# Kernel tuning notes

Hardware: AMD Instinct MI355X
Metric: run time of the kernel (lower is better)

Reference implementation:

```python
import math
import jax, jax.numpy as jnp
import numpy as np

D = 768      # hidden_size
H = 16       # num_attention_heads (hardcoded in module)
DH = D // H  # value dim per head
SEQ = 512    # fpos/tpos are taken modulo 512
EPS = 1e-5   # torch LayerNorm default
SCALE = math.sqrt(D / H)  # attention_head_size = dim_key_query_all / num_heads


def _collab_attn(h, fpos, tpos, Wq, Wk, Wcb, Wv, bv, mix, Wd, bd, lng, lnb):
    """CollaborativeAttention.forward on one segment. h: [SEQ, D]."""
    fpos = fpos % SEQ
    tpos = tpos % SEQ
    fs = h[fpos]                                   # [F, D] gathered 'from' nodes
    ts = h[tpos]                                   # [T, D] gathered 'to' nodes
    q = fs @ Wq.T                                  # [F, D] (no bias)
    k = ts @ Wk.T                                  # [T, D] (no bias)
    mq = q[None, :, :] * mix[:, None, :]           # [H, F, D] per-head mixing
    scores = jnp.einsum('hfd,td->hft', mq, k)      # [H, F, T] full-D contraction
    cb = (ts @ Wcb.T).T                            # [H, T] content bias
    scores = (scores + cb[:, None, :]) / SCALE
    probs = jax.nn.softmax(scores, axis=-1)        # dropout = identity at eval
    v = (ts @ Wv.T + bv).reshape(-1, H, DH).transpose(1, 0, 2)  # [H, T, DH]
    ctx = jnp.einsum('hft,htd->hfd', probs, v)     # [H, F, DH]
    ctx = ctx.transpose(1, 0, 2).reshape(-1, D) @ Wd.T + bd      # [F, D]
    x = fs + ctx                                   # residual on gathered nodes
    mu = x.mean(-1, keepdims=True)
    var = ((x - mu) ** 2).mean(-1, keepdims=True)
    return lng * (x - mu) / jnp.sqrt(var + EPS) + lnb


def _encoder(hidden_states, fpos, tpos, qtoc, ctoq):
    outs = []
    for b in range(3):  # fixed small segment count, matches original unrolling
        o1 = _collab_attn(hidden_states[b], fpos[b], tpos[b], *qtoc).mean(0)
        o2 = _collab_attn(hidden_states[b], tpos[b], fpos[b], *ctoq).mean(0)
        outs.append(jnp.concatenate([o1, o2]))
    return jnp.stack(outs)  # [3, 2*D]


def setup_inputs() -> dict:
    key = jax.random.key(0)
    ks = jax.random.split(key, 32)
    inp = {
        'hidden_states': jax.random.normal(ks[0], (3, SEQ, D), jnp.float32),
        'fpos': jax.random.randint(ks[1], (3, 2048), 0, SEQ, jnp.int32),
        'tpos': jax.random.randint(ks[2], (3, 2048), 0, SEQ, jnp.int32),
    }
    i = 3
    for p in ('qtoc', 'ctoq'):
        for n, shape, std in (('Wq', (D, D), 0.02), ('Wk', (D, D), 0.02),
                              ('Wcb', (H, D), 0.02), ('Wv', (D, D), 0.02),
                              ('Wd', (D, D), 0.02), ('mix', (H, D), 0.2)):
            inp[p + '_' + n] = std * jax.random.normal(ks[i], shape, jnp.float32)
            i += 1
        inp[p + '_bv'] = jnp.zeros((D,), jnp.float32)
        inp[p + '_bd'] = jnp.zeros((D,), jnp.float32)
        inp[p + '_lng'] = jnp.ones((D,), jnp.float32)
        inp[p + '_lnb'] = jnp.zeros((D,), jnp.float32)
    return inp


def reference(hidden_states, fpos, tpos,
              qtoc_Wq, qtoc_Wk, qtoc_Wcb, qtoc_Wv, qtoc_Wd, qtoc_mix,
              qtoc_bv, qtoc_bd, qtoc_lng, qtoc_lnb,
              ctoq_Wq, ctoq_Wk, ctoq_Wcb, ctoq_Wv, ctoq_Wd, ctoq_mix,
              ctoq_bv, ctoq_bd, ctoq_lng, ctoq_lnb):
    qtoc = (qtoc_Wq, qtoc_Wk, qtoc_Wcb, qtoc_Wv, qtoc_bv, qtoc_mix,
            qtoc_Wd, qtoc_bd, qtoc_lng, qtoc_lnb)
    ctoq = (ctoq_Wq, ctoq_Wk, ctoq_Wcb, ctoq_Wv, ctoq_bv, ctoq_mix,
            ctoq_Wd, ctoq_bd, ctoq_lng, ctoq_lnb)
    return _encoder(hidden_states, fpos, tpos, qtoc, ctoq)
```

## Files before the change

kernel.cpp:

```cpp
#include <hip/hip_runtime.h>
#include <math.h>

#define DD 768
#define HH 16
#define DHH 48
#define NPOS 512
#define NIDX 2048
#define INV_SCALE 0.14433756729740643f
#define LN_EPS 1e-5f

typedef __bf16 bf16_t;
typedef __bf16 bf16x8 __attribute__((ext_vector_type(8)));
typedef float f32x4 __attribute__((ext_vector_type(4)));

__device__ __forceinline__ void g2lds16(const void* g, void* l) {
  __builtin_amdgcn_global_load_lds((const __attribute__((address_space(1))) void*)g,
                                   (__attribute__((address_space(3))) void*)l, 16, 0, 0);
}

struct CvtDesc { const float* src; bf16_t* dst; int n8; };
struct CvtBatch { CvtDesc d[9]; };

__global__ __launch_bounds__(256) void prep(const int* __restrict__ fpos,
                                            const int* __restrict__ tpos,
                                            int* __restrict__ CNT, CvtBatch cvb,
                                            const float* __restrict__ hs,
                                            const float* __restrict__ Wcb0,
                                            const float* __restrict__ Wcb1,
                                            float* __restrict__ cbG) {
  const int bid = blockIdx.x;
  const int tid = threadIdx.x;
  __shared__ int shist[NPOS];
  if (bid < 6) {
    const int b = bid >> 1, which = bid & 1;
    const int* src = (which ? tpos : fpos) + b * NIDX;
    for (int i = tid; i < NPOS; i += 256) shist[i] = 0;
    __syncthreads();
    for (int i = tid; i < NIDX; i += 256) atomicAdd(&shist[src[i] & (NPOS - 1)], 1);
    __syncthreads();
    for (int i = tid; i < NPOS; i += 256) CNT[bid * NPOS + i] = shist[i];
  } else if (bid < 582) {
    const CvtDesc de = cvb.d[(bid - 6) >> 6];
    for (int i = ((bid - 6) & 63) * 256 + tid; i < de.n8; i += 64 * 256) {
      const f32x4 a = *(const f32x4*)(de.src + (size_t)i * 8);
      const f32x4 b = *(const f32x4*)(de.src + (size_t)i * 8 + 4);
      bf16_t t[8];
#pragma unroll
      for (int e = 0; e < 4; ++e) { t[e] = (bf16_t)a[e]; t[4 + e] = (bf16_t)b[e]; }
      *(bf16x8*)(de.dst + (size_t)i * 8) = *(bf16x8*)t;
    }
  } else {
    const int g = bid - 582;
    const int pd = g >> 5, t0 = (g & 31) * 16;
    const int b = pd >> 1;
    const float* W = (pd & 1) ? Wcb1 : Wcb0;
    const int tl = tid >> 4, hh = tid & 15;
    const float* hrow = hs + ((size_t)b * NPOS + t0 + tl) * DD;
    const float* wrow = W + hh * DD;
    float s = 0.f;
    for (int k = 0; k < DD; k += 4) {
      const f32x4 a = *(const f32x4*)(hrow + k);
      const f32x4 bq = *(const f32x4*)(wrow + k);
      s += a[0] * bq[0] + a[1] * bq[1] + a[2] * bq[2] + a[3] * bq[3];
    }
    cbG[((size_t)pd * NPOS + t0 + tl) * HH + hh] = s;
  }
}

struct MDesc { const bf16_t* A; const bf16_t* B; const float* bias; void* C; int out_bf16; };
struct MBatch { MDesc d[18]; };

__global__ __launch_bounds__(256, 2) void mfma_gemm(MBatch batch) {
  const MDesc de = batch.d[blockIdx.y];
  const int mt = blockIdx.x & 3, nt = blockIdx.x >> 2;
  const int m0 = mt * 128, n0 = nt * 128;

  __shared__ bf16_t At[4096];
  __shared__ bf16_t Bt[4096];

  const int tid = threadIdx.x;
  const int w = tid >> 6, lane = tid & 63;
  const int wm = w >> 1, wn = w & 1;
  const int lm = lane & 15, lq = lane >> 4;

  f32x4 acc[4][4] = {};

  for (int k0 = 0; k0 < 768; k0 += 32) {
    __syncthreads();
    {
      const int lqq = lane & 3, lr = lane >> 2;
#pragma unroll
      for (int i = 0; i < 2; ++i) {
        const int issue = w + i * 4;
        const int row = issue * 16 + lr;
        g2lds16(de.A + (size_t)(m0 + row) * 768 + k0 + lqq * 8, At + issue * 512);
        g2lds16(de.B + (size_t)(n0 + row) * 768 + k0 + lqq * 8, Bt + issue * 512);
      }
    }
    __syncthreads();
    bf16x8 af[4], bfr[4];
#pragma unroll
    for (int f = 0; f < 4; ++f) {
      af[f] = *(const bf16x8*)(At + (wm * 64 + f * 16 + lm) * 32 + lq * 8);
      bfr[f] = *(const bf16x8*)(Bt + (wn * 64 + f * 16 + lm) * 32 + lq * 8);
    }
#pragma unroll
    for (int i = 0; i < 4; ++i)
#pragma unroll
      for (int j = 0; j < 4; ++j)
        acc[i][j] = __builtin_amdgcn_mfma_f32_16x16x32_bf16(af[i], bfr[j], acc[i][j], 0, 0, 0);
  }

#pragma unroll
  for (int i = 0; i < 4; ++i) {
    const int rbase = m0 + wm * 64 + i * 16 + lq * 4;
#pragma unroll
    for (int j = 0; j < 4; ++j) {
      const int c = n0 + wn * 64 + j * 16 + lm;
      const float bv = de.bias ? de.bias[c] : 0.f;
#pragma unroll
      for (int r = 0; r < 4; ++r) {
        const float v = acc[i][j][r] + bv;
        if (de.out_bf16) ((bf16_t*)de.C)[(size_t)(rbase + r) * 768 + c] = (bf16_t)v;
        else             ((float*)de.C)[(size_t)(rbase + r) * 768 + c] = v;
      }
    }
  }
}

__global__ __launch_bounds__(256) void vtrans(const bf16_t* __restrict__ V,
                                              bf16_t* __restrict__ Vt) {
  const int g = blockIdx.x;
  const int tt = g & 15;
  const int rem = g >> 4;
  const int dt = rem % 24, pd = rem / 24;
  const int t0 = tt * 32, d0 = dt * 32;
  __shared__ bf16_t tile[32][34];
  const int c = threadIdx.x & 31, r0 = threadIdx.x >> 5;
#pragma unroll
  for (int i = 0; i < 4; ++i) {
    const int r = r0 + i * 8;
    tile[c][r] = V[((size_t)pd * NPOS + t0 + r) * DD + d0 + c];
  }
  __syncthreads();
#pragma unroll
  for (int i = 0; i < 4; ++i) {
    const int r = r0 + i * 8;
    Vt[((size_t)pd * DD + d0 + r) * NPOS + t0 + c] = tile[r][c];
  }
}

__global__ __launch_bounds__(256, 3) void attn_mfma(
    const bf16_t* __restrict__ Qg, const bf16_t* __restrict__ Kg,
    const bf16_t* __restrict__ Vt, const float* __restrict__ cbG,
    const int* __restrict__ CNT, const float* __restrict__ mix0,
    const float* __restrict__ mix1, bf16_t* __restrict__ CTX) {
  const int bid = blockIdx.x;
  const int ft = bid & 7, h = (bid >> 3) & 15, pd = bid >> 7;
  const int dir = pd & 1;
  const int f0 = ft * 64;

  __shared__ bf16_t At[64 * 32];
  __shared__ bf16_t Bt[128 * 32];
  __shared__ bf16_t P[64 * 136];
  __shared__ bf16_t Vs[64 * 136];
  __shared__ float mixs[768];
  __shared__ float cbw[512];
  __shared__ float rowl[64];

  const int tid = threadIdx.x;
  const int w = tid >> 6, lane = tid & 63;
  const bf16_t* Qp = Qg + (size_t)pd * NPOS * DD;
  const bf16_t* Kp = Kg + (size_t)pd * NPOS * DD;
  const bf16_t* Vp = Vt + (size_t)pd * DD * NPOS + (size_t)h * DHH * NPOS;
  const float* mix = (dir ? mix1 : mix0) + h * DD;
  const int* cnt = CNT + ((pd & ~1) + (1 - dir)) * NPOS;

  for (int i = tid; i < 768; i += 256) mixs[i] = mix[i];
  for (int i = tid; i < 512; i += 256)
    cbw[i] = cbG[((size_t)pd * NPOS + i) * HH + h] * INV_SCALE + __logf((float)cnt[i]);
  for (int i = tid; i < 16 * 136; i += 256) {
    const int r = i / 136, c = i % 136;
    Vs[(48 + r) * 136 + c] = (bf16_t)((r == 0 && c < 128) ? 1.f : 0.f);
  }
  __syncthreads();

  const int wm = w >> 1, wn = w & 1;
  const int lm = lane & 15, lq = lane >> 4;
  const int sr = lane >> 2, sq = lane & 3;

  f32x4 pv[4] = {};

  for (int jt = 0; jt < 4; ++jt) {
    const int j0 = jt * 128;
    f32x4 sa[2][4] = {};

    for (int k0 = 0; k0 < DD; k0 += 32) {
      __syncthreads();
#pragma unroll
      for (int c = 0; c < 3; ++c) {
        const int issue = w + c * 4;
        if (issue < 4)
          g2lds16(Qp + (size_t)(f0 + issue * 16 + sr) * DD + k0 + sq * 8, At + issue * 512);
        else {
          const int e = issue - 4;
          g2lds16(Kp + (size_t)(j0 + e * 16 + sr) * DD + k0 + sq * 8, Bt + e * 512);
        }
      }
      __syncthreads();
      const f32x4 mxa = *(const f32x4*)&mixs[k0 + lq * 8];
      const f32x4 mxb = *(const f32x4*)&mixs[k0 + lq * 8 + 4];
      bf16x8 af[2], bfr[4];
#pragma unroll
      for (int i = 0; i < 2; ++i) {
        const bf16x8 q = *(const bf16x8*)(At + (wm * 32 + i * 16 + lm) * 32 + lq * 8);
        bf16_t t[8];
#pragma unroll
        for (int e = 0; e < 4; ++e) {
          t[e]     = (bf16_t)((float)q[e] * mxa[e]);
          t[4 + e] = (bf16_t)((float)q[4 + e] * mxb[e]);
        }
        af[i] = *(bf16x8*)t;
      }
#pragma unroll
      for (int j = 0; j < 4; ++j)
        bfr[j] = *(const bf16x8*)(Bt + (wn * 64 + j * 16 + lm) * 32 + lq * 8);
#pragma unroll
      for (int i = 0; i < 2; ++i)
#pragma unroll
        for (int j = 0; j < 4; ++j)
          sa[i][j] = __builtin_amdgcn_mfma_f32_16x16x32_bf16(af[i], bfr[j], sa[i][j], 0, 0, 0);
    }
    __syncthreads();

#pragma unroll
    for (int j = 0; j < 4; ++j) {
      const int col = wn * 64 + j * 16 + lm;
      const float cb = cbw[j0 + col];
#pragma unroll
      for (int i = 0; i < 2; ++i) {
        const int rbase = wm * 32 + i * 16 + lq * 4;
#pragma unroll
        for (int r = 0; r < 4; ++r)
          P[(rbase + r) * 136 + col] = (bf16_t)__expf(sa[i][j][r] * INV_SCALE + cb);
      }
    }
    for (int i = tid; i < 48 * 16; i += 256) {
      const int r = i >> 4, cc = i & 15;
      *(bf16x8*)(Vs + r * 136 + cc * 8) = *(const bf16x8*)(Vp + (size_t)r * NPOS + j0 + cc * 8);
    }
    __syncthreads();

#pragma unroll
    for (int kk = 0; kk < 4; ++kk) {
      const bf16x8 pa = *(const bf16x8*)(P + (w * 16 + lm) * 136 + kk * 32 + lq * 8);
#pragma unroll
      for (int j = 0; j < 4; ++j) {
        const bf16x8 pb = *(const bf16x8*)(Vs + (j * 16 + lm) * 136 + kk * 32 + lq * 8);
        pv[j] = __builtin_amdgcn_mfma_f32_16x16x32_bf16(pa, pb, pv[j], 0, 0, 0);
      }
    }
  }

  if (lm == 0) {
#pragma unroll
    for (int r = 0; r < 4; ++r) rowl[w * 16 + lq * 4 + r] = pv[3][r];
  }
  __syncthreads();
#pragma unroll
  for (int j = 0; j < 3; ++j) {
#pragma unroll
    for (int r = 0; r < 4; ++r) {
      const int fr = w * 16 + lq * 4 + r;
      CTX[((size_t)pd * NPOS + f0 + fr) * DD + h * DHH + j * 16 + lm] =
          (bf16_t)(pv[j][r] / rowl[fr]);
    }
  }
}

__global__ __launch_bounds__(256) void ln_mean_kernel(
    const float* __restrict__ hs, const float* __restrict__ XB,
    const int* __restrict__ CNT,
    const float* __restrict__ lng0, const float* __restrict__ lnb0,
    const float* __restrict__ lng1, const float* __restrict__ lnb1,
    float* __restrict__ out) {
  const int blk = blockIdx.x;
  const int chunk = blk & 15;
  const int pd = blk >> 4;
  const int b = pd >> 1, dir = pd & 1;
  const float* lng = dir ? lng1 : lng0;
  const float* lnb = dir ? lnb1 : lnb0;
  const int* cnt = CNT + pd * NPOS;
  const float* hb = hs + (size_t)b * NPOS * DD;
  const float* xb = XB + (size_t)pd * NPOS * DD;

  __shared__ float wacc[4][DD];
  const int tid = threadIdx.x;
  const int wave = tid >> 6, lane = tid & 63;
  for (int d0 = tid; d0 < 4 * DD; d0 += 256) ((float*)wacc)[d0] = 0.f;
  __syncthreads();

  float lg[12], lb[12];
#pragma unroll
  for (int qd = 0; qd < 12; ++qd) {
    lg[qd] = lng[lane + qd * 64];
    lb[qd] = lnb[lane + qd * 64];
  }

  for (int rr = 0; rr < 8; ++rr) {
    const int p = chunk * 32 + wave * 8 + rr;
    float x[12];
    float s = 0.f, ss = 0.f;
#pragma unroll
    for (int qd = 0; qd < 12; ++qd) {
      const int d0 = lane + qd * 64;
      const float xv = hb[(size_t)p * DD + d0] + xb[(size_t)p * DD + d0];
      x[qd] = xv; s += xv; ss += xv * xv;
    }
#pragma unroll
    for (int o = 1; o < 64; o <<= 1) {
      s += __shfl_xor(s, o);
      ss += __shfl_xor(ss, o);
    }
    const float mu = s * (1.f / 768.f);
    const float var = ss * (1.f / 768.f) - mu * mu;
    const float rstd = rsqrtf(var + LN_EPS);
    const float wgt = (float)cnt[p];
    if (wgt != 0.f) {
#pragma unroll
      for (int qd = 0; qd < 12; ++qd) {
        const int d0 = lane + qd * 64;
        wacc[wave][d0] += wgt * (lg[qd] * (x[qd] - mu) * rstd + lb[qd]);
      }
    }
  }
  __syncthreads();
  for (int d0 = tid; d0 < DD; d0 += 256) {
    const float t = wacc[0][d0] + wacc[1][d0] + wacc[2][d0] + wacc[3][d0];
    atomicAdd(&out[b * 1536 + dir * 768 + d0], t * (1.f / 2048.f));
  }
}

extern "C" void kernel_launch(void* const* d_in, const int* in_sizes, int n_in,
                              void* d_out, int out_size, void* d_ws, size_t ws_size,
                              hipStream_t stream) {
  const float* hs  = (const float*)d_in[0];
  const int* fpos  = (const int*)d_in[1];
  const int* tpos  = (const int*)d_in[2];

  const float* Wq[2]; const float* Wk[2]; const float* Wcb[2]; const float* Wv[2];
  const float* Wd[2]; const float* mixp[2];
  const float* bv[2]; const float* bd[2]; const float* lng[2]; const float* lnb[2];
  for (int p = 0; p < 2; ++p) {
    const int base = 3 + p * 10;
    Wq[p]   = (const float*)d_in[base + 0];
    Wk[p]   = (const float*)d_in[base + 1];
    Wcb[p]  = (const float*)d_in[base + 2];
    Wv[p]   = (const float*)d_in[base + 3];
    Wd[p]   = (const float*)d_in[base + 4];
    mixp[p] = (const float*)d_in[base + 5];
    bv[p]   = (const float*)d_in[base + 6];
    bd[p]   = (const float*)d_in[base + 7];
    lng[p]  = (const float*)d_in[base + 8];
    lnb[p]  = (const float*)d_in[base + 9];
  }

  char* wsp = (char*)d_ws;
  size_t off = 0;
  auto alloc = [&](size_t bytes) { char* p = wsp + off; off = (off + bytes + 255) & ~(size_t)255; return p; };
  bf16_t* hsb  = (bf16_t*)alloc((size_t)3 * NPOS * DD * 2);
  bf16_t* Wb   = (bf16_t*)alloc((size_t)8 * DD * DD * 2);
  bf16_t* Qbf  = (bf16_t*)alloc((size_t)6 * NPOS * DD * 2);
  bf16_t* Kbf  = (bf16_t*)alloc((size_t)6 * NPOS * DD * 2);
  bf16_t* Vbf  = (bf16_t*)alloc((size_t)6 * NPOS * DD * 2);
  bf16_t* VtG  = (bf16_t*)alloc((size_t)6 * DD * NPOS * 2);
  bf16_t* CTXb = (bf16_t*)alloc((size_t)6 * NPOS * DD * 2);
  float*  XB   = (float*) alloc((size_t)6 * NPOS * DD * 4);
  float*  cbG  = (float*) alloc((size_t)6 * NPOS * HH * 4);
  int*    CNTb = (int*)   alloc((size_t)6 * NPOS * 4);

  hipMemsetAsync(d_out, 0, (size_t)out_size * sizeof(float), stream);

  CvtBatch cvb{};
  cvb.d[0] = CvtDesc{hs, hsb, 3 * NPOS * DD / 8};
  const float* wsrc[8] = {Wq[0], Wk[0], Wv[0], Wd[0], Wq[1], Wk[1], Wv[1], Wd[1]};
  for (int i = 0; i < 8; ++i)
    cvb.d[1 + i] = CvtDesc{wsrc[i], Wb + (size_t)i * DD * DD, DD * DD / 8};
  prep<<<774, 256, 0, stream>>>(fpos, tpos, CNTb, cvb, hs, Wcb[0], Wcb[1], cbG);

  MBatch gb{};
  int n = 0;
  for (int b = 0; b < 3; ++b)
    for (int p = 0; p < 2; ++p) {
      const int pd = b * 2 + p;
      const bf16_t* A = hsb + (size_t)b * NPOS * DD;
      const size_t o = (size_t)pd * NPOS * DD;
      gb.d[n++] = MDesc{A, Wb + (size_t)(p * 4 + 0) * DD * DD, nullptr, Qbf + o, 1};
      gb.d[n++] = MDesc{A, Wb + (size_t)(p * 4 + 1) * DD * DD, nullptr, Kbf + o, 1};
      gb.d[n++] = MDesc{A, Wb + (size_t)(p * 4 + 2) * DD * DD, bv[p],   Vbf + o, 1};
    }
  mfma_gemm<<<dim3(24, 18), 256, 0, stream>>>(gb);

  vtrans<<<2304, 256, 0, stream>>>(Vbf, VtG);

  attn_mfma<<<768, 256, 0, stream>>>(Qbf, Kbf, VtG, cbG, CNTb, mixp[0], mixp[1], CTXb);

  MBatch gd{};
  for (int b = 0; b < 3; ++b)
    for (int p = 0; p < 2; ++p) {
      const int pd = b * 2 + p;
      const size_t o = (size_t)pd * NPOS * DD;
      gd.d[pd] = MDesc{CTXb + o, Wb + (size_t)(p * 4 + 3) * DD * DD, bd[p], XB + o, 0};
    }
  mfma_gemm<<<dim3(24, 6), 256, 0, stream>>>(gd);

  ln_mean_kernel<<<96, 256, 0, stream>>>(hs, XB, CNTb, lng[0], lnb[0], lng[1], lnb[1],
                                         (float*)d_out);
}
```

Measured before the change: 286.1 us.

## Double-buffer GEMM and attention loads, fuse V transpose, shrink tiles and LDS

The GEMM tile shrinks to 64x128 and both GEMM and attention score loops now double-buffer their global-to-LDS loads, issuing the next k-slice before computing the current one. The V projection writes its output already transposed, which removes the separate vtrans kernel and the Vbf buffer. Attention LDS is packed into one union buffer, allowing 4 blocks per CU, and the softmax scale is folded into the mix vector. The aim is to hide load latency, raise occupancy and cut one launch plus a memory round-trip, at the cost of strided scattered stores for the transposed V output.

```diff
diff --git a/kernel.cpp b/kernel.cpp
--- a/kernel.cpp
+++ b/kernel.cpp
@@ -67,53 +67,62 @@
   }
 }
 
-struct MDesc { const bf16_t* A; const bf16_t* B; const float* bias; void* C; int out_bf16; };
+struct MDesc { const bf16_t* A; const bf16_t* B; const float* bias; void* C; int mode; };
 struct MBatch { MDesc d[18]; };
 
-__global__ __launch_bounds__(256, 2) void mfma_gemm(MBatch batch) {
+__global__ __launch_bounds__(256, 4) void gemm64(MBatch batch) {
   const MDesc de = batch.d[blockIdx.y];
-  const int mt = blockIdx.x & 3, nt = blockIdx.x >> 2;
-  const int m0 = mt * 128, n0 = nt * 128;
-
-  __shared__ bf16_t At[4096];
-  __shared__ bf16_t Bt[4096];
+  const int mt = blockIdx.x & 7, nt = blockIdx.x >> 3;
+  const int m0 = mt * 64, n0 = nt * 128;
+
+  __shared__ bf16_t SA[2][2048];
+  __shared__ bf16_t SB[2][4096];
 
   const int tid = threadIdx.x;
   const int w = tid >> 6, lane = tid & 63;
   const int wm = w >> 1, wn = w & 1;
   const int lm = lane & 15, lq = lane >> 4;
-
-  f32x4 acc[4][4] = {};
-
-  for (int k0 = 0; k0 < 768; k0 += 32) {
-    __syncthreads();
-    {
-      const int lqq = lane & 3, lr = lane >> 2;
-#pragma unroll
-      for (int i = 0; i < 2; ++i) {
-        const int issue = w + i * 4;
-        const int row = issue * 16 + lr;
-        g2lds16(de.A + (size_t)(m0 + row) * 768 + k0 + lqq * 8, At + issue * 512);
-        g2lds16(de.B + (size_t)(n0 + row) * 768 + k0 + lqq * 8, Bt + issue * 512);
-      }
-    }
-    __syncthreads();
-    bf16x8 af[4], bfr[4];
-#pragma unroll
-    for (int f = 0; f < 4; ++f) {
-      af[f] = *(const bf16x8*)(At + (wm * 64 + f * 16 + lm) * 32 + lq * 8);
-      bfr[f] = *(const bf16x8*)(Bt + (wn * 64 + f * 16 + lm) * 32 + lq * 8);
-    }
-#pragma unroll
-    for (int i = 0; i < 4; ++i)
+  const int sr = lane >> 2, sq = lane & 3;
+
+  f32x4 acc[2][4] = {};
+
+  auto stage = [&](int buf, int k0) {
+#pragma unroll
+    for (int c = 0; c < 3; ++c) {
+      const int issue = w + c * 4;
+      if (issue < 4)
+        g2lds16(de.A + (size_t)(m0 + issue * 16 + sr) * 768 + k0 + sq * 8,
+                SA[buf] + issue * 512);
+      else {
+        const int e = issue - 4;
+        g2lds16(de.B + (size_t)(n0 + e * 16 + sr) * 768 + k0 + sq * 8,
+                SB[buf] + e * 512);
+      }
+    }
+  };
+
+  stage(0, 0);
+  for (int k0i = 0; k0i < 24; ++k0i) {
+    const int cur = k0i & 1;
+    __syncthreads();
+    if (k0i + 1 < 24) stage(cur ^ 1, (k0i + 1) * 32);
+    bf16x8 af[2], bfr[4];
+#pragma unroll
+    for (int i = 0; i < 2; ++i)
+      af[i] = *(const bf16x8*)(SA[cur] + (wm * 32 + i * 16 + lm) * 32 + lq * 8);
+#pragma unroll
+    for (int j = 0; j < 4; ++j)
+      bfr[j] = *(const bf16x8*)(SB[cur] + (wn * 64 + j * 16 + lm) * 32 + lq * 8);
+#pragma unroll
+    for (int i = 0; i < 2; ++i)
 #pragma unroll
       for (int j = 0; j < 4; ++j)
         acc[i][j] = __builtin_amdgcn_mfma_f32_16x16x32_bf16(af[i], bfr[j], acc[i][j], 0, 0, 0);
   }
 
 #pragma unroll
-  for (int i = 0; i < 4; ++i) {
-    const int rbase = m0 + wm * 64 + i * 16 + lq * 4;
+  for (int i = 0; i < 2; ++i) {
+    const int rbase = m0 + wm * 32 + i * 16 + lq * 4;
 #pragma unroll
     for (int j = 0; j < 4; ++j) {
       const int c = n0 + wn * 64 + j * 16 + lm;
@@ -121,36 +130,15 @@
 #pragma unroll
       for (int r = 0; r < 4; ++r) {
         const float v = acc[i][j][r] + bv;
-        if (de.out_bf16) ((bf16_t*)de.C)[(size_t)(rbase + r) * 768 + c] = (bf16_t)v;
-        else             ((float*)de.C)[(size_t)(rbase + r) * 768 + c] = v;
-      }
-    }
-  }
-}
-
-__global__ __launch_bounds__(256) void vtrans(const bf16_t* __restrict__ V,
-                                              bf16_t* __restrict__ Vt) {
-  const int g = blockIdx.x;
-  const int tt = g & 15;
-  const int rem = g >> 4;
-  const int dt = rem % 24, pd = rem / 24;
-  const int t0 = tt * 32, d0 = dt * 32;
-  __shared__ bf16_t tile[32][34];
-  const int c = threadIdx.x & 31, r0 = threadIdx.x >> 5;
-#pragma unroll
-  for (int i = 0; i < 4; ++i) {
-    const int r = r0 + i * 8;
-    tile[c][r] = V[((size_t)pd * NPOS + t0 + r) * DD + d0 + c];
-  }
-  __syncthreads();
-#pragma unroll
-  for (int i = 0; i < 4; ++i) {
-    const int r = r0 + i * 8;
-    Vt[((size_t)pd * DD + d0 + r) * NPOS + t0 + c] = tile[r][c];
-  }
-}
-
-__global__ __launch_bounds__(256, 3) void attn_mfma(
+        if (de.mode == 0)      ((float*)de.C)[(size_t)(rbase + r) * 768 + c] = v;
+        else if (de.mode == 1) ((bf16_t*)de.C)[(size_t)(rbase + r) * 768 + c] = (bf16_t)v;
+        else                   ((bf16_t*)de.C)[(size_t)c * NPOS + rbase + r] = (bf16_t)v;
+      }
+    }
+  }
+}
+
+__global__ __launch_bounds__(256, 4) void attn_mfma(
     const bf16_t* __restrict__ Qg, const bf16_t* __restrict__ Kg,
     const bf16_t* __restrict__ Vt, const float* __restrict__ cbG,
     const int* __restrict__ CNT, const float* __restrict__ mix0,
@@ -160,10 +148,7 @@
   const int dir = pd & 1;
   const int f0 = ft * 64;
 
-  __shared__ bf16_t At[64 * 32];
-  __shared__ bf16_t Bt[128 * 32];
-  __shared__ bf16_t P[64 * 136];
-  __shared__ bf16_t Vs[64 * 136];
+  __shared__ bf16_t U[17408];
   __shared__ float mixs[768];
   __shared__ float cbw[512];
   __shared__ float rowl[64];
@@ -176,14 +161,9 @@
   const float* mix = (dir ? mix1 : mix0) + h * DD;
   const int* cnt = CNT + ((pd & ~1) + (1 - dir)) * NPOS;
 
-  for (int i = tid; i < 768; i += 256) mixs[i] = mix[i];
+  for (int i = tid; i < 768; i += 256) mixs[i] = mix[i] * INV_SCALE;
   for (int i = tid; i < 512; i += 256)
     cbw[i] = cbG[((size_t)pd * NPOS + i) * HH + h] * INV_SCALE + __logf((float)cnt[i]);
-  for (int i = tid; i < 16 * 136; i += 256) {
-    const int r = i / 136, c = i % 136;
-    Vs[(48 + r) * 136 + c] = (bf16_t)((r == 0 && c < 128) ? 1.f : 0.f);
-  }
-  __syncthreads();
 
   const int wm = w >> 1, wn = w & 1;
   const int lm = lane & 15, lq = lane >> 4;
@@ -193,27 +173,36 @@
 
   for (int jt = 0; jt < 4; ++jt) {
     const int j0 = jt * 128;
-    f32x4 sa[2][4] = {};
-
-    for (int k0 = 0; k0 < DD; k0 += 32) {
-      __syncthreads();
+    __syncthreads();
+
+    auto stage = [&](int buf, int k0) {
 #pragma unroll
       for (int c = 0; c < 3; ++c) {
         const int issue = w + c * 4;
         if (issue < 4)
-          g2lds16(Qp + (size_t)(f0 + issue * 16 + sr) * DD + k0 + sq * 8, At + issue * 512);
+          g2lds16(Qp + (size_t)(f0 + issue * 16 + sr) * DD + k0 + sq * 8,
+                  U + buf * 6144 + issue * 512);
         else {
           const int e = issue - 4;
-          g2lds16(Kp + (size_t)(j0 + e * 16 + sr) * DD + k0 + sq * 8, Bt + e * 512);
+          g2lds16(Kp + (size_t)(j0 + e * 16 + sr) * DD + k0 + sq * 8,
+                  U + buf * 6144 + 2048 + e * 512);
         }
       }
+    };
+
+    stage(0, 0);
+    f32x4 sa[2][4] = {};
+    for (int k0i = 0; k0i < 24; ++k0i) {
+      const int cur = k0i & 1;
+      const int k0 = k0i * 32;
       __syncthreads();
+      if (k0i + 1 < 24) stage(cur ^ 1, k0 + 32);
       const f32x4 mxa = *(const f32x4*)&mixs[k0 + lq * 8];
       const f32x4 mxb = *(const f32x4*)&mixs[k0 + lq * 8 + 4];
       bf16x8 af[2], bfr[4];
 #pragma unroll
       for (int i = 0; i < 2; ++i) {
-        const bf16x8 q = *(const bf16x8*)(At + (wm * 32 + i * 16 + lm) * 32 + lq * 8);
+        const bf16x8 q = *(const bf16x8*)(U + cur * 6144 + (wm * 32 + i * 16 + lm) * 32 + lq * 8);
         bf16_t t[8];
 #pragma unroll
         for (int e = 0; e < 4; ++e) {
@@ -224,7 +213,7 @@
       }
 #pragma unroll
       for (int j = 0; j < 4; ++j)
-        bfr[j] = *(const bf16x8*)(Bt + (wn * 64 + j * 16 + lm) * 32 + lq * 8);
+        bfr[j] = *(const bf16x8*)(U + cur * 6144 + 2048 + (wn * 64 + j * 16 + lm) * 32 + lq * 8);
 #pragma unroll
       for (int i = 0; i < 2; ++i)
 #pragma unroll
@@ -242,21 +231,29 @@
         const int rbase = wm * 32 + i * 16 + lq * 4;
 #pragma unroll
         for (int r = 0; r < 4; ++r)
-          P[(rbase + r) * 136 + col] = (bf16_t)__expf(sa[i][j][r] * INV_SCALE + cb);
-      }
-    }
-    for (int i = tid; i < 48 * 16; i += 256) {
+          U[(rbase + r) * 136 + col] = (bf16_t)__expf(sa[i][j][r] + cb);
+      }
+    }
+    for (int i = tid; i < 49 * 16; i += 256) {
       const int r = i >> 4, cc = i & 15;
-      *(bf16x8*)(Vs + r * 136 + cc * 8) = *(const bf16x8*)(Vp + (size_t)r * NPOS + j0 + cc * 8);
+      if (r < 48)
+        *(bf16x8*)(U + 8704 + r * 136 + cc * 8) =
+            *(const bf16x8*)(Vp + (size_t)r * NPOS + j0 + cc * 8);
+      else {
+        bf16_t ones[8];
+#pragma unroll
+        for (int e = 0; e < 8; ++e) ones[e] = (bf16_t)1.f;
+        *(bf16x8*)(U + 8704 + 48 * 136 + cc * 8) = *(bf16x8*)ones;
+      }
     }
     __syncthreads();
 
 #pragma unroll
     for (int kk = 0; kk < 4; ++kk) {
-      const bf16x8 pa = *(const bf16x8*)(P + (w * 16 + lm) * 136 + kk * 32 + lq * 8);
+      const bf16x8 pa = *(const bf16x8*)(U + (w * 16 + lm) * 136 + kk * 32 + lq * 8);
 #pragma unroll
       for (int j = 0; j < 4; ++j) {
-        const bf16x8 pb = *(const bf16x8*)(Vs + (j * 16 + lm) * 136 + kk * 32 + lq * 8);
+        const bf16x8 pb = *(const bf16x8*)(U + 8704 + (j * 16 + lm) * 136 + kk * 32 + lq * 8);
         pv[j] = __builtin_amdgcn_mfma_f32_16x16x32_bf16(pa, pb, pv[j], 0, 0, 0);
       }
     }
@@ -372,7 +369,6 @@
   bf16_t* Wb   = (bf16_t*)alloc((size_t)8 * DD * DD * 2);
   bf16_t* Qbf  = (bf16_t*)alloc((size_t)6 * NPOS * DD * 2);
   bf16_t* Kbf  = (bf16_t*)alloc((size_t)6 * NPOS * DD * 2);
-  bf16_t* Vbf  = (bf16_t*)alloc((size_t)6 * NPOS * DD * 2);
   bf16_t* VtG  = (bf16_t*)alloc((size_t)6 * DD * NPOS * 2);
   bf16_t* CTXb = (bf16_t*)alloc((size_t)6 * NPOS * DD * 2);
   float*  XB   = (float*) alloc((size_t)6 * NPOS * DD * 4);
@@ -397,11 +393,9 @@
       const size_t o = (size_t)pd * NPOS * DD;
       gb.d[n++] = MDesc{A, Wb + (size_t)(p * 4 + 0) * DD * DD, nullptr, Qbf + o, 1};
       gb.d[n++] = MDesc{A, Wb + (size_t)(p * 4 + 1) * DD * DD, nullptr, Kbf + o, 1};
-      gb.d[n++] = MDesc{A, Wb + (size_t)(p * 4 + 2) * DD * DD, bv[p],   Vbf + o, 1};
-    }
-  mfma_gemm<<<dim3(24, 18), 256, 0, stream>>>(gb);
-
-  vtrans<<<2304, 256, 0, stream>>>(Vbf, VtG);
+      gb.d[n++] = MDesc{A, Wb + (size_t)(p * 4 + 2) * DD * DD, bv[p],   VtG + (size_t)pd * DD * NPOS, 2};
+    }
+  gemm64<<<dim3(48, 18), 256, 0, stream>>>(gb);
 
   attn_mfma<<<768, 256, 0, stream>>>(Qbf, Kbf, VtG, cbG, CNTb, mixp[0], mixp[1], CTXb);
 
@@ -412,7 +406,7 @@
       const size_t o = (size_t)pd * NPOS * DD;
       gd.d[pd] = MDesc{CTXb + o, Wb + (size_t)(p * 4 + 3) * DD * DD, bd[p], XB + o, 0};
     }
-  mfma_gemm<<<dim3(24, 6), 256, 0, stream>>>(gd);
+  gemm64<<<dim3(48, 6), 256, 0, stream>>>(gd);
 
   ln_mean_kernel<<<96, 256, 0, stream>>>(hs, XB, CNTb, lng[0], lnb[0], lng[1], lnb[1],
                                          (float*)d_out);
```

Result: no change. 288.2 us (+0.8%).
